# Kernel tuning notes

Hardware: AMD Instinct MI355X
Metric: run time of the kernel (lower is better)

The kernel has to match this reference:

```python
import jax, jax.numpy as jnp
import numpy as np

V_MIN = -10.0
V_MAX = 10.0
NUM_ATOMS = 51
ATOM_DELTA = (V_MAX - V_MIN) / (NUM_ATOMS - 1)
BS = 1_000_000


def setup_inputs() -> dict:
    key = jax.random.key(0)
    k1, k2 = jax.random.split(key)
    reward = jax.random.normal(k1, (BS,), dtype=jnp.float32) * 3.0
    probs = jax.random.uniform(k2, (BS, NUM_ATOMS), dtype=jnp.float32)
    atom_values = (V_MIN + ATOM_DELTA * jnp.arange(NUM_ATOMS)).astype(jnp.float32)
    return {"reward": reward, "probs": probs, "atom_values": atom_values}


def reference(reward, probs, atom_values):
    # Categorical (C51) Bellman projection, expressed as a scatter-add
    # instead of the original's dense [bs, A, A] projection matrix + bmm.
    bs, A = probs.shape
    # shifted & clamped atom support: [bs, A]
    new_vals = jnp.clip(atom_values[None, :] + reward[:, None], V_MIN, V_MAX)
    idx = (new_vals - V_MIN) / ATOM_DELTA           # fractional atom index
    lower = jnp.floor(idx)
    upper = jnp.ceil(idx)
    same = lower == upper                           # idx landed exactly on an atom
    l_coef = jnp.where(same, 1.0, upper - idx)      # original sets 1.0 when l == u
    u_coef = idx - lower                            # 0 when same
    li = lower.astype(jnp.int32)
    ui = upper.astype(jnp.int32)
    rows = jnp.broadcast_to(jnp.arange(bs)[:, None], (bs, A))
    out = jnp.zeros_like(probs)
    out = out.at[rows, li].add(l_coef * probs)
    out = out.at[rows, ui].add(u_coef * probs)
    return out
```

## Files before the change

kernel.cpp:

```cpp
#include <hip/hip_runtime.h>

#define NA 51
#define ROWS 64
#define GUARD 56
#define NDATA (ROWS * NA)
#define BUFSZ (GUARD + NDATA + GUARD)
#define KCLAMP 52
#define NBLK 1536

typedef float v4 __attribute__((ext_vector_type(4), aligned(16)));

#define WAITV(N) do { asm volatile("s_waitcnt vmcnt(" #N ")" ::: "memory"); \
                      __builtin_amdgcn_sched_barrier(0); } while (0)

__global__ __launch_bounds__(ROWS, 2) void c51_bellman_kernel(
    const float* __restrict__ reward,
    const float* __restrict__ probs,
    float* __restrict__ out,
    int bs)
{
    __shared__ __align__(16) float bufA[BUFSZ];
    __shared__ __align__(16) float bufB[BUFSZ];
    float* const dA = bufA + GUARD;
    float* const dB = bufB + GUARD;
    const int tid   = threadIdx.x;
    const int gs    = gridDim.x;
    const int nfull = bs / ROWS;
    const int rem   = bs - nfull * ROWS;

    auto issueL = [&](long tile, float* dst) {
        const char* src = (const char*)probs + (size_t)tile * (NDATA * 4);
        #pragma unroll
        for (int c = 0; c < 12; ++c) {
            __builtin_amdgcn_global_load_lds(
                (const __attribute__((address_space(1))) void*)
                    (unsigned long long)(src + c * 1024 + tid * 16),
                (__attribute__((address_space(3))) void*)
                    (unsigned long long)(dst + c * 256),
                16, 0, 0);
        }
        if (tid < 48) {
            __builtin_amdgcn_global_load_lds(
                (const __attribute__((address_space(1))) void*)
                    (unsigned long long)(src + 12288 + tid * 16),
                (__attribute__((address_space(3))) void*)
                    (unsigned long long)(dst + 3072),
                16, 0, 0);
        }
    };

    auto computeT = [&](float* data, float rw) {
        const float s  = rw * 2.5f;
        const float kf = floorf(s);
        const float f  = s - kf;
        int k = (int)kf;
        k = min(max(k, -KCLAMP), KCLAMP);
        const float* rp = data + tid * NA;

        float m_lo = 0.0f, m_hi = 0.0f;
        #pragma unroll
        for (int j = 0; j < NA; ++j) {
            const float pj = rp[j];
            const float t  = (float)j + s;
            if (t < 0.0f)  m_lo += pj;
            if (t > 50.0f) m_hi += pj;
        }

        const float* wb = rp - k - 1;
        float w[52];
        #pragma unroll
        for (int m = 0; m < 52; ++m) w[m] = wb[m];

        float* wp = data + tid * NA;
        const float w1 = 1.0f - f;
        float prev = ((unsigned)(-k - 1) <= 50u) ? w[0] : 0.0f;
        #pragma unroll
        for (int i = 0; i < NA; ++i) {
            const float cur = ((unsigned)(i - k) <= 50u) ? w[i + 1] : 0.0f;
            float o;
            if (i == 0)           o = w1 * cur + m_lo;
            else if (i == NA - 1) o = ((f == 0.0f) ? cur : f * prev) + m_hi;
            else                  o = w1 * cur + f * prev;
            wp[i] = o;
            prev = cur;
        }
    };

    auto storeT = [&](const float* data, long tile) {
        const v4* l4 = (const v4*)data;
        v4* o4 = (v4*)(out + (size_t)tile * NDATA);
        #pragma unroll
        for (int m = 0; m < 12; ++m)
            o4[m * 64 + tid] = l4[m * 64 + tid];
        if (tid < 48)
            o4[768 + tid] = l4[768 + tid];
    };

    long t = blockIdx.x;
    if (t < nfull) {
        float rwA = reward[t * ROWS + tid];
        issueL(t, dA);
        for (;;) {
            const long tB = t + gs;
            const bool hB = tB < nfull;
            float rwB = 0.0f;
            if (hB) { rwB = reward[tB * ROWS + tid]; issueL(tB, dB); WAITV(14); }
            else    { WAITV(0); }
            computeT(dA, rwA);
            storeT(dA, t);
            if (!hB) break;

            const long tA2 = tB + gs;
            const bool hA = tA2 < nfull;
            if (hA) { rwA = reward[tA2 * ROWS + tid]; issueL(tA2, dA); WAITV(14); }
            else    { WAITV(0); }
            computeT(dB, rwB);
            storeT(dB, tB);
            if (!hA) break;
            t = tA2;
        }
    }

    if (rem && blockIdx.x == 0) {
        const int r = nfull * ROWS + tid;
        if (r < bs) {
            const float s  = reward[r] * 2.5f;
            const float kf = floorf(s);
            const float f  = s - kf;
            int k = (int)kf; k = min(max(k, -KCLAMP), KCLAMP);
            const float* rp = probs + (size_t)r * NA;
            float row[NA];
            #pragma unroll
            for (int j = 0; j < NA; ++j) row[j] = rp[j];
            float m_lo = 0.0f, m_hi = 0.0f;
            #pragma unroll
            for (int j = 0; j < NA; ++j) {
                const float tt = (float)j + s;
                if (tt < 0.0f)  m_lo += row[j];
                if (tt > 50.0f) m_hi += row[j];
            }
            float w[52];
            #pragma unroll
            for (int m = 0; m < 52; ++m)
                w[m] = row[min(max(m - k - 1, 0), NA - 1)];
            float* op = out + (size_t)r * NA;
            const float w1 = 1.0f - f;
            float prev = ((unsigned)(-k - 1) <= 50u) ? w[0] : 0.0f;
            #pragma unroll
            for (int i = 0; i < NA; ++i) {
                const float cur = ((unsigned)(i - k) <= 50u) ? w[i + 1] : 0.0f;
                float o;
                if (i == 0)           o = w1 * cur + m_lo;
                else if (i == NA - 1) o = ((f == 0.0f) ? cur : f * prev) + m_hi;
                else                  o = w1 * cur + f * prev;
                op[i] = o;
                prev = cur;
            }
        }
    }
}

extern "C" void kernel_launch(void* const* d_in, const int* in_sizes, int n_in,
                              void* d_out, int out_size, void* d_ws, size_t ws_size,
                              hipStream_t stream) {
    const float* reward = (const float*)d_in[0];
    const float* probs  = (const float*)d_in[1];
    float* out = (float*)d_out;
    const int bs = in_sizes[0];

    const int nfull = bs / ROWS;
    int blocks = nfull < NBLK ? nfull : NBLK;
    if (blocks < 1) blocks = 1;
    c51_bellman_kernel<<<blocks, ROWS, 0, stream>>>(reward, probs, out, bs);
}
```

Before: 393.7 us.

## Replace LDS double buffer with register prefetch and single LDS tile

Instead of double-buffering tiles in LDS with global_load_lds, each thread prefetches the next tile's probabilities and reward into 13 vector registers while the current tile is computed and stored. The prefetched registers are then written into a single LDS buffer. This halves LDS per block and raises the grid cap from 1536 to 2048 blocks, aiming for more resident waves to hide memory latency. The cost is extra register pressure on top of the existing 52-float window, plus an extra register-to-LDS copy per tile.

```diff
diff --git a/kernel.cpp b/kernel.cpp
--- a/kernel.cpp
+++ b/kernel.cpp
@@ -6,7 +6,7 @@
 #define NDATA (ROWS * NA)
 #define BUFSZ (GUARD + NDATA + GUARD)
 #define KCLAMP 52
-#define NBLK 1536
+#define NBLK 2048
 
 typedef float v4 __attribute__((ext_vector_type(4), aligned(16)));
 
@@ -19,37 +19,31 @@
     float* __restrict__ out,
     int bs)
 {
-    __shared__ __align__(16) float bufA[BUFSZ];
-    __shared__ __align__(16) float bufB[BUFSZ];
-    float* const dA = bufA + GUARD;
-    float* const dB = bufB + GUARD;
+    __shared__ __align__(16) float buf[BUFSZ];
+    float* const data = buf + GUARD;
     const int tid   = threadIdx.x;
     const int gs    = gridDim.x;
     const int nfull = bs / ROWS;
     const int rem   = bs - nfull * ROWS;
 
-    auto issueL = [&](long tile, float* dst) {
-        const char* src = (const char*)probs + (size_t)tile * (NDATA * 4);
+    v4 pf[13];
+    float rwPf = 0.0f;
+
+    auto issuePF = [&](long tile) {
+        const v4* s4 = (const v4*)(probs + (size_t)tile * NDATA);
         #pragma unroll
-        for (int c = 0; c < 12; ++c) {
-            __builtin_amdgcn_global_load_lds(
-                (const __attribute__((address_space(1))) void*)
-                    (unsigned long long)(src + c * 1024 + tid * 16),
-                (__attribute__((address_space(3))) void*)
-                    (unsigned long long)(dst + c * 256),
-                16, 0, 0);
-        }
-        if (tid < 48) {
-            __builtin_amdgcn_global_load_lds(
-                (const __attribute__((address_space(1))) void*)
-                    (unsigned long long)(src + 12288 + tid * 16),
-                (__attribute__((address_space(3))) void*)
-                    (unsigned long long)(dst + 3072),
-                16, 0, 0);
-        }
+        for (int c = 0; c < 12; ++c) pf[c] = s4[c * 64 + tid];
+        if (tid < 48) pf[12] = s4[768 + tid];
+        rwPf = reward[tile * ROWS + tid];
+    };
+    auto writePF = [&]() {
+        v4* d4 = (v4*)data;
+        #pragma unroll
+        for (int c = 0; c < 12; ++c) d4[c * 64 + tid] = pf[c];
+        if (tid < 48) d4[768 + tid] = pf[12];
     };
 
-    auto computeT = [&](float* data, float rw) {
+    auto computeT = [&](float rw) {
         const float s  = rw * 2.5f;
         const float kf = floorf(s);
         const float f  = s - kf;
@@ -86,7 +80,7 @@
         }
     };
 
-    auto storeT = [&](const float* data, long tile) {
+    auto storeT = [&](long tile) {
         const v4* l4 = (const v4*)data;
         v4* o4 = (v4*)(out + (size_t)tile * NDATA);
         #pragma unroll
@@ -98,26 +92,21 @@
 
     long t = blockIdx.x;
     if (t < nfull) {
-        float rwA = reward[t * ROWS + tid];
-        issueL(t, dA);
+        issuePF(t);
+        WAITV(0);
+        writePF();
+        float rwCur = rwPf;
         for (;;) {
-            const long tB = t + gs;
-            const bool hB = tB < nfull;
-            float rwB = 0.0f;
-            if (hB) { rwB = reward[tB * ROWS + tid]; issueL(tB, dB); WAITV(14); }
-            else    { WAITV(0); }
-            computeT(dA, rwA);
-            storeT(dA, t);
-            if (!hB) break;
-
-            const long tA2 = tB + gs;
-            const bool hA = tA2 < nfull;
-            if (hA) { rwA = reward[tA2 * ROWS + tid]; issueL(tA2, dA); WAITV(14); }
-            else    { WAITV(0); }
-            computeT(dB, rwB);
-            storeT(dB, tB);
-            if (!hA) break;
-            t = tA2;
+            const long tn = t + gs;
+            const bool hN = tn < nfull;
+            if (hN) issuePF(tn);
+            computeT(rwCur);
+            storeT(t);
+            if (!hN) break;
+            WAITV(13);
+            writePF();
+            rwCur = rwPf;
+            t = tn;
         }
     }
 
```

Result: faster. 351.0 us (-10.8%).
